# Kernel optimization log

Measured on AMD Instinct MI355X. Metric: run time of the kernel, lower is better.

Reference implementation:

```python
import jax, jax.numpy as jnp
import numpy as np

PI = 3.1415927410125732
N = 4096
VELOCITY = 5e-7
RC = 3.15e-6          # collision radius
RR = 8e-6             # repulsion radius
RO = 2.5e-5           # orientation radius (Ra = inf -> inside_Ra all-true)
ALPHA = PI            # field of view; < 2*pi so within_view masking is active
DT_TRANS = 1.4e-14    # translational diffusion DT
DR = 0.0028
GAMMA = 25.0
DT = 0.2              # timestep dt
COLLISION_ITERS = 3   # fixed-iteration version of recursive solve_collisions
EPS = 1e-14


def _c(x):  # [N,2] real -> complex64
    return jax.lax.complex(x[..., 0], x[..., 1])


def _r(z):  # complex -> [..., 2] real
    return jnp.stack([z.real, z.imag], axis=-1)


def _anglediff(a, b):
    # torch get_anglediff: wrap angle(a)-angle(b) into (-pi, pi)
    diff = jnp.angle(a) - jnp.angle(b)
    diff = jnp.where(diff <= -PI, jnp.mod(diff, PI), diff)
    return diff - (diff >= PI) * (2.0 * PI)


def _cossim(a, b):
    # nn.CosineSimilarity(dim=1, eps=1e-14) on view_as_real of complex vectors
    dot = a.real * b.real + a.imag * b.imag
    na = jnp.sqrt(a.real ** 2 + a.imag ** 2 + 1e-30)
    nb = jnp.sqrt(b.real ** 2 + b.imag ** 2 + 1e-30)
    return dot / (jnp.maximum(na, EPS) * jnp.maximum(nb, EPS))


def setup_inputs() -> dict:
    key = jax.random.key(0)
    k1, k2, k3, k4, k5 = jax.random.split(key, 5)
    positions = jax.random.normal(k1, (N, 2), jnp.float32) * 5e-4
    ang = jax.random.uniform(k2, (N,), jnp.float32, -PI, PI)
    orientations = jnp.stack([jnp.cos(ang), jnp.sin(ang)], axis=-1)  # unit complex
    Deltas = jax.random.uniform(k3, (1,), jnp.float32, 0.1, 0.6)
    rot_noise = jax.random.normal(k4, (N,), jnp.float32)
    trans_noise = jax.random.normal(k5, (N, 2), jnp.float32)
    return {"positions": positions, "orientations": orientations, "Deltas": Deltas,
            "rot_noise": rot_noise, "trans_noise": trans_noise}


def reference(positions, orientations, Deltas, rot_noise, trans_noise):
    p = _c(positions)      # [N] complex positions
    u = _c(orientations)   # [N] complex orientations
    n = p.shape[0]
    eye = jnp.eye(n, dtype=bool)

    # pairwise direction/distance: dirs[i,j] = p_j - p_i
    dirs = p[None, :] - p[:, None]
    dists = jnp.abs(dirs)

    inside_Rr = (dists <= RR) & ~eye
    inside_Ro = dists <= RO + RC
    # inside_Ra with Ra = inf is all-True

    # angle between separation vector and orientation of the *neighbor* j
    ang_diff = _anglediff(dirs, u[None, :])
    in_front = ang_diff < PI / 2
    within_view = ang_diff < ALPHA  # alpha < 2*pi branch active

    cdtype = p.dtype
    mask_rr = (inside_Rr & in_front).astype(cdtype)
    mask_ra = within_view.astype(cdtype)  # inside_Ra all True
    mask_ro = (inside_Ro & within_view).astype(cdtype)

    n_r = mask_rr.real.sum(axis=1)
    S = (mask_rr @ p) / jnp.maximum(n_r, 1.0) - p * jnp.sign(n_r)
    d = -S

    n_a = mask_ra.real.sum(axis=1)
    cms = (mask_ra @ p) / jnp.maximum(n_a, 1.0)
    Ps = cms - p * jnp.sign(n_a)

    orientation_sums = mask_ro @ u

    leftturns = Ps * jnp.exp(1j * Deltas)
    rightturns = Ps * jnp.exp(-1j * Deltas)

    # T >= T_release branch: pick the turn most aligned with neighbor orientations
    left_closer = _cossim(leftturns, orientation_sums) >= _cossim(rightturns, orientation_sums)
    best_turns = jnp.where(left_closer, leftturns, rightturns)

    d_abs = jnp.abs(d)
    d_safe = jnp.where(d_abs > 0, d, jnp.ones((), cdtype))
    best_safe = jnp.where(jnp.abs(best_turns) > 0, best_turns, jnp.ones((), cdtype))
    angle_to_target = jnp.where(d_abs > 0, _anglediff(d_safe, u), _anglediff(best_safe, u))

    # rotational_noise = randn * sqrt(2*DR); rotation = exp(i*(dt*Gamma*DR*sin + noise*sqrt(dt)))
    rot = jnp.exp(1j * (DT * GAMMA * DR * jnp.sin(angle_to_target)
                        + rot_noise * np.float32(np.sqrt(2 * DR)) * np.float32(np.sqrt(DT))))

    # complex-normal translational noise (per-component std 1/sqrt(2)) * sqrt(2*DT) * sqrt(dt)
    tn = _c(trans_noise) * np.float32(np.sqrt(0.5)) * np.float32(np.sqrt(2 * DT_TRANS))
    translation = DT * VELOCITY * u + tn * np.float32(np.sqrt(DT))

    def collide(i, pos):
        dd = pos[None, :] - pos[:, None]
        dd_nd = jnp.where(eye, jnp.ones((), pos.dtype), dd)  # avoid 0/0 on diagonal
        ab = jnp.where(eye, 0.0, jnp.abs(dd_nd))
        coll = ab <= 2 * RC - jnp.eye(n, dtype=ab.dtype)
        safe = jnp.where(coll, ab, 1.0)
        move = jnp.where(coll, dd / safe * ((2.1 * RC - ab) * 0.5), jnp.zeros((), pos.dtype))
        return pos - move.sum(axis=1)

    new_p = jax.lax.fori_loop(0, COLLISION_ITERS, collide, p + translation)
    new_u = u * rot

    # pack the 5 complex outputs as real [5, N, 2]
    return jnp.stack([_r(new_p), _r(new_u), _r(orientation_sums), _r(leftturns), _r(rightturns)], axis=0)
```

## Files before the change

### kernel.cpp

```cpp
#include <hip/hip_runtime.h>
#include <math.h>

#define NPART 4096
#define NBLK  512
#define NTHR  256
#define IPB   8
#define CAPL  1024
#define SMAX  512

constexpr float RORC   = (float)(2.5e-5 + 3.15e-6);
constexpr float RORC2  = RORC * RORC;
constexpr float RRF    = 8e-6f;
constexpr float RR2    = RRF * RRF;
constexpr float TWORC  = (float)(2.0 * 3.15e-6);
constexpr float TWORC2 = TWORC * TWORC;
constexpr float C21RC  = (float)(2.1 * 3.15e-6);
constexpr float RCAND2 = 1.6e-9f;
constexpr float C_ROT  = (float)(0.2 * 25.0 * 0.0028);
constexpr float C_RN1  = (float)0.07483314773547883;
constexpr float C_SQDT = (float)0.4472135954999579;
constexpr float C_TRV  = (float)(0.2 * 5e-7);
constexpr float C_HALF = (float)0.7071067811865476;
constexpr float C_SQ2T = (float)1.6733200530681511e-07;
constexpr float EPSF   = 1e-14f;

__global__ __launch_bounds__(NTHR) void fused_all(
        const float2* __restrict__ pos, const float2* __restrict__ ori,
        const float* __restrict__ Deltas, const float* __restrict__ rot_noise,
        const float2* __restrict__ trans_noise, float2* __restrict__ out) {
    __shared__ float4   pp4[NPART / 2];
    __shared__ float    sred[2 * NTHR];
    __shared__ float    res[5][IPB];
    __shared__ unsigned bmap[NPART / 32];
    __shared__ int      lpairs[CAPL];
    __shared__ int      Sidx[SMAX];
    __shared__ float4   posS4[SMAX / 2];
    __shared__ int      lcnt, scnt;
    __shared__ int      iloc[IPB];
    float2* ppos_s = (float2*)pp4;
    float2* posS   = (float2*)posS4;

    const int tid = threadIdx.x;
    if (tid == 0) { lcnt = 0; scnt = 0; }
    if (tid < 5 * IPB) ((float*)res)[tid] = 0.f;
    if (tid < NPART / 32) bmap[tid] = 0u;
    const int il  = tid & (IPB - 1);
    const int seg = tid / IPB;
    const int gi  = blockIdx.x * IPB + il;

    for (int k = 0; k < NPART / NTHR; ++k)
        ppos_s[k * NTHR + tid] = pos[k * NTHR + tid];
    __syncthreads();

    const float2 pi = ppos_s[gi];
    const int base64 = seg * 64;
    for (int tb = 0; tb < 16; ++tb) {
        const int kb = (tb + seg) & 15;
        const float4 v0 = pp4[base64 + kb];
        const float4 v1 = pp4[base64 + kb + 16];
        const float4 v2 = pp4[base64 + kb + 32];
        const float4 v3 = pp4[base64 + kb + 48];
        #pragma unroll
        for (int s = 0; s < 4; ++s) {
            const float4 v = (s == 0) ? v0 : (s == 1) ? v1 : (s == 2) ? v2 : v3;
            const int j0 = seg * 128 + 2 * (kb + 16 * s);
            const float dx0 = v.x - pi.x, dy0 = v.y - pi.y;
            const float dx1 = v.z - pi.x, dy1 = v.w - pi.y;
            const float r20 = fmaf(dx0, dx0, dy0 * dy0);
            const float r21 = fmaf(dx1, dx1, dy1 * dy1);
            if (fminf(r20, r21) <= RCAND2) {
                if (r20 <= RCAND2) {
                    const int slot = atomicAdd(&lcnt, 1);
                    if (slot < CAPL) lpairs[slot] = (il << 12) | j0;
                    atomicOr(&bmap[j0 >> 5], 1u << (j0 & 31));
                }
                if (r21 <= RCAND2) {
                    const int j1 = j0 + 1;
                    const int slot = atomicAdd(&lcnt, 1);
                    if (slot < CAPL) lpairs[slot] = (il << 12) | j1;
                    atomicOr(&bmap[j1 >> 5], 1u << (j1 & 31));
                }
            }
        }
    }
    __syncthreads();

    const int n_l = (lcnt < CAPL) ? lcnt : CAPL;
    if (tid < 128) {
        for (int e = tid; e < n_l; e += 128) {
            const int code = lpairs[e];
            const int jil = code >> 12, j = code & (NPART - 1);
            const float2 pj = ppos_s[j];
            const float2 pi2 = ppos_s[blockIdx.x * IPB + jil];
            const float dx = pj.x - pi2.x, dy = pj.y - pi2.y;
            const float r2 = fmaf(dx, dx, dy * dy);
            if (r2 <= RORC2) {
                const float2 uj = ori[j];
                atomicAdd(&res[3][jil], uj.x);
                atomicAdd(&res[4][jil], uj.y);
                if (r2 <= RR2 && r2 > 0.f) {
                    const float dt_ = fmaf(dx, uj.x, dy * uj.y);
                    const float cr_ = fmaf(dy, uj.x, -dx * uj.y);
                    if (!((dt_ <= 0.f) && (cr_ >= 0.f))) {
                        atomicAdd(&res[0][jil], 1.f);
                        atomicAdd(&res[1][jil], pj.x);
                        atomicAdd(&res[2][jil], pj.y);
                    }
                }
            }
        }
    } else {
        const int w = tid - 128;
        unsigned bits = bmap[w];
        while (bits) {
            const int b = __ffs(bits) - 1;
            bits &= bits - 1;
            const int p = w * 32 + b;
            const int slot = atomicAdd(&scnt, 1);
            if (slot < SMAX) {
                Sidx[slot] = p;
                if ((p >> 3) == (int)blockIdx.x) iloc[p & (IPB - 1)] = slot;
            }
        }
    }
    __syncthreads();
    const int nS = (scnt < SMAX) ? scnt : SMAX;

    for (int m = tid; m < nS; m += NTHR) {
        const int p = Sidx[m];
        const float2 pp = ppos_s[p];
        const float2 uu = ori[p];
        const float2 tn = trans_noise[p];
        posS[m] = make_float2(
            pp.x + (C_TRV * uu.x + ((tn.x * C_HALF) * C_SQ2T) * C_SQDT),
            pp.y + (C_TRV * uu.y + ((tn.y * C_HALF) * C_SQ2T) * C_SQDT));
    }

    float mx = 0.f, my = 0.f;
    for (int k = 0; k < NPART / NTHR; ++k) {
        const float2 v = ppos_s[k * NTHR + tid];
        mx += v.x; my += v.y;
    }
    sred[tid] = mx; sred[NTHR + tid] = my;
    __syncthreads();
    for (int s = NTHR / 2; s > 0; s >>= 1) {
        if (tid < s) { sred[tid] += sred[tid + s]; sred[NTHR + tid] += sred[NTHR + tid + s]; }
        __syncthreads();
    }
    const float cmx = sred[0]    * (1.f / NPART);
    const float cmy = sred[NTHR] * (1.f / NPART);

    if (tid < IPB) {
        const int g2 = blockIdx.x * IPB + tid;
        const float2 p = ppos_s[g2];
        const float2 u = ori[g2];
        const float nrv = res[0][tid], sxv = res[1][tid], syv = res[2][tid];
        const float osx = res[3][tid], osy = res[4][tid];

        const float inv = 1.f / fmaxf(nrv, 1.f);
        const float sg  = (nrv > 0.f) ? 1.f : 0.f;
        const float Sx = sxv * inv - p.x * sg;
        const float Sy = syv * inv - p.y * sg;
        const float dxv = -Sx, dyv = -Sy;

        const float Psx = cmx - p.x;
        const float Psy = cmy - p.y;

        float sd, cd;
        sincosf(Deltas[0], &sd, &cd);
        const float Lx = Psx * cd - Psy * sd;
        const float Ly = Psx * sd + Psy * cd;
        const float Rx = Psx * cd + Psy * sd;
        const float Ry = Psy * cd - Psx * sd;

        const float no  = fmaxf(sqrtf(osx * osx + osy * osy + 1e-30f), EPSF);
        const float nl  = fmaxf(sqrtf(Lx * Lx + Ly * Ly + 1e-30f), EPSF);
        const float nrr = fmaxf(sqrtf(Rx * Rx + Ry * Ry + 1e-30f), EPSF);
        const float csl = (Lx * osx + Ly * osy) / (nl * no);
        const float csr = (Rx * osx + Ry * osy) / (nrr * no);
        const bool left = (csl >= csr);
        const float bx = left ? Lx : Rx;
        const float by = left ? Ly : Ry;

        float cx, cy;
        if (dxv != 0.f || dyv != 0.f)    { cx = dxv; cy = dyv; }
        else if (bx != 0.f || by != 0.f) { cx = bx;  cy = by;  }
        else                             { cx = 1.f; cy = 0.f; }

        const float dt_ = cx * u.x + cy * u.y;
        const float cr_ = cy * u.x - cx * u.y;
        const float sin_t = cr_ / sqrtf(dt_ * dt_ + cr_ * cr_);

        const float ang = C_ROT * sin_t + (rot_noise[g2] * C_RN1) * C_SQDT;
        float sa, ca;
        sincosf(ang, &sa, &ca);
        out[1 * NPART + g2] = make_float2(u.x * ca - u.y * sa,
                                          u.x * sa + u.y * ca);
        out[2 * NPART + g2] = make_float2(osx, osy);
        out[3 * NPART + g2] = make_float2(Lx, Ly);
        out[4 * NPART + g2] = make_float2(Rx, Ry);
    }
    __syncthreads();

    for (int pass = 0; pass < 3; ++pass) {
        float px[2], py[2], ax[2] = {0.f, 0.f}, ay[2] = {0.f, 0.f};
        bool  mv[2];
        #pragma unroll
        for (int q = 0; q < 2; ++q) {
            const int m = tid + q * NTHR;
            mv[q] = (m < nS);
            if (mv[q]) { px[q] = posS[m].x; py[q] = posS[m].y; }
        }
        int b = 0;
        for (; b + 4 <= nS; b += 4) {
            const float4 w0 = posS4[(b >> 1)];
            const float4 w1 = posS4[(b >> 1) + 1];
            const float bxs[4] = {w0.x, w0.z, w1.x, w1.z};
            const float bys[4] = {w0.y, w0.w, w1.y, w1.w};
            #pragma unroll
            for (int s = 0; s < 4; ++s) {
                #pragma unroll
                for (int q = 0; q < 2; ++q) {
                    if (mv[q]) {
                        const float dx = bxs[s] - px[q], dy = bys[s] - py[q];
                        const float r2 = fmaf(dx, dx, dy * dy);
                        if (r2 <= TWORC2 && r2 > 0.f) {
                            const float ab = sqrtf(r2);
                            const float sc = (C21RC - ab) * 0.5f / ab;
                            ax[q] = fmaf(dx, sc, ax[q]);
                            ay[q] = fmaf(dy, sc, ay[q]);
                        }
                    }
                }
            }
        }
        for (; b < nS; ++b) {
            const float2 pb = posS[b];
            #pragma unroll
            for (int q = 0; q < 2; ++q) {
                if (mv[q]) {
                    const float dx = pb.x - px[q], dy = pb.y - py[q];
                    const float r2 = fmaf(dx, dx, dy * dy);
                    if (r2 <= TWORC2 && r2 > 0.f) {
                        const float ab = sqrtf(r2);
                        const float sc = (C21RC - ab) * 0.5f / ab;
                        ax[q] = fmaf(dx, sc, ax[q]);
                        ay[q] = fmaf(dy, sc, ay[q]);
                    }
                }
            }
        }
        __syncthreads();
        #pragma unroll
        for (int q = 0; q < 2; ++q) {
            const int m = tid + q * NTHR;
            if (m < nS) posS[m] = make_float2(px[q] - ax[q], py[q] - ay[q]);
        }
        __syncthreads();
    }
    if (tid < IPB)
        out[0 * NPART + blockIdx.x * IPB + tid] = posS[iloc[tid]];
}

extern "C" void kernel_launch(void* const* d_in, const int* in_sizes, int n_in,
                              void* d_out, int out_size, void* d_ws, size_t ws_size,
                              hipStream_t stream) {
    const float2* pos = (const float2*)d_in[0];
    const float2* ori = (const float2*)d_in[1];
    const float*  del = (const float*)d_in[2];
    const float*  rn  = (const float*)d_in[3];
    const float2* tn  = (const float2*)d_in[4];
    float2* o2 = (float2*)d_out;
    (void)d_ws; (void)ws_size;

    fused_all<<<dim3(NBLK), dim3(NTHR), 0, stream>>>(pos, ori, del, rn, tn, o2);
}
```

Baseline: 96.23 us.

## Replace brute-force neighbor scan with per-block uniform grid cell list

Each block now bins all 4096 particles into a 64x64 uniform grid in shared memory (count, scan, scatter) and then checks only the 3x3 neighbouring cells of each of its 8 particles, one warp-sized group per particle. This replaces the all-pairs scan of 4096 candidates per particle and the shared pair list with atomic accumulation. Each block rebuilds the full grid redundantly, which adds atomics, a block scan and extra syncs. The cell size must be at least the candidate radius, and particles outside the grid extent are clamped into the edge cells.

```diff
diff --git a/kernel.cpp b/kernel.cpp
--- a/kernel.cpp
+++ b/kernel.cpp
@@ -5,8 +5,9 @@
 #define NBLK  512
 #define NTHR  256
 #define IPB   8
-#define CAPL  1024
 #define SMAX  512
+#define GDIM  64
+#define NCELL (GDIM * GDIM)
 
 constexpr float RORC   = (float)(2.5e-5 + 3.15e-6);
 constexpr float RORC2  = RORC * RORC;
@@ -16,6 +17,8 @@
 constexpr float TWORC2 = TWORC * TWORC;
 constexpr float C21RC  = (float)(2.1 * 3.15e-6);
 constexpr float RCAND2 = 1.6e-9f;
+constexpr float GMIN   = -2.048e-3f;
+constexpr float GINV   = 15625.0f;
 constexpr float C_ROT  = (float)(0.2 * 25.0 * 0.0028);
 constexpr float C_RN1  = (float)0.07483314773547883;
 constexpr float C_SQDT = (float)0.4472135954999579;
@@ -24,92 +27,133 @@
 constexpr float C_SQ2T = (float)1.6733200530681511e-07;
 constexpr float EPSF   = 1e-14f;
 
+__device__ __forceinline__ int cell_of(float x, float y) {
+    int cx = (int)floorf((x - GMIN) * GINV);
+    int cy = (int)floorf((y - GMIN) * GINV);
+    cx = min(max(cx, 0), GDIM - 1);
+    cy = min(max(cy, 0), GDIM - 1);
+    return cy * GDIM + cx;
+}
+
 __global__ __launch_bounds__(NTHR) void fused_all(
         const float2* __restrict__ pos, const float2* __restrict__ ori,
         const float* __restrict__ Deltas, const float* __restrict__ rot_noise,
         const float2* __restrict__ trans_noise, float2* __restrict__ out) {
     __shared__ float4   pp4[NPART / 2];
-    __shared__ float    sred[2 * NTHR];
+    __shared__ int      ptr[NCELL];
+    __shared__ unsigned short sortid[NPART];
+    __shared__ float    sred[5 * NTHR];
     __shared__ float    res[5][IPB];
     __shared__ unsigned bmap[NPART / 32];
-    __shared__ int      lpairs[CAPL];
     __shared__ int      Sidx[SMAX];
     __shared__ float4   posS4[SMAX / 2];
-    __shared__ int      lcnt, scnt;
+    __shared__ int      scnt;
     __shared__ int      iloc[IPB];
     float2* ppos_s = (float2*)pp4;
     float2* posS   = (float2*)posS4;
-
-    const int tid = threadIdx.x;
-    if (tid == 0) { lcnt = 0; scnt = 0; }
-    if (tid < 5 * IPB) ((float*)res)[tid] = 0.f;
+    int*    sredi  = (int*)sred;
+
+    const int tid  = threadIdx.x;
+    const int il   = tid >> 5;
+    const int lane = tid & 31;
+    const int gi   = blockIdx.x * IPB + il;
+    if (tid == 0) scnt = 0;
     if (tid < NPART / 32) bmap[tid] = 0u;
-    const int il  = tid & (IPB - 1);
-    const int seg = tid / IPB;
-    const int gi  = blockIdx.x * IPB + il;
 
     for (int k = 0; k < NPART / NTHR; ++k)
         ppos_s[k * NTHR + tid] = pos[k * NTHR + tid];
+    for (int k = 0; k < NCELL / NTHR; ++k)
+        ptr[k * NTHR + tid] = 0;
+    __syncthreads();
+
+    for (int k = 0; k < NPART / NTHR; ++k) {
+        const int p = k * NTHR + tid;
+        const float2 pp = ppos_s[p];
+        atomicAdd(&ptr[cell_of(pp.x, pp.y)], 1);
+    }
+    __syncthreads();
+
+    {
+        const int base = tid * (NCELL / NTHR);
+        int v[NCELL / NTHR];
+        int sum = 0;
+        #pragma unroll
+        for (int t = 0; t < NCELL / NTHR; ++t) { v[t] = ptr[base + t]; sum += v[t]; }
+        sredi[tid] = sum;
+        __syncthreads();
+        for (int off = 1; off < NTHR; off <<= 1) {
+            const int a = (tid >= off) ? sredi[tid - off] : 0;
+            __syncthreads();
+            sredi[tid] += a;
+            __syncthreads();
+        }
+        int run = sredi[tid] - sum;
+        #pragma unroll
+        for (int t = 0; t < NCELL / NTHR; ++t) { ptr[base + t] = run; run += v[t]; }
+    }
+    __syncthreads();
+
+    for (int k = 0; k < NPART / NTHR; ++k) {
+        const int p = k * NTHR + tid;
+        const float2 pp = ppos_s[p];
+        const int slot = atomicAdd(&ptr[cell_of(pp.x, pp.y)], 1);
+        sortid[slot] = (unsigned short)p;
+    }
     __syncthreads();
 
     const float2 pi = ppos_s[gi];
-    const int base64 = seg * 64;
-    for (int tb = 0; tb < 16; ++tb) {
-        const int kb = (tb + seg) & 15;
-        const float4 v0 = pp4[base64 + kb];
-        const float4 v1 = pp4[base64 + kb + 16];
-        const float4 v2 = pp4[base64 + kb + 32];
-        const float4 v3 = pp4[base64 + kb + 48];
-        #pragma unroll
-        for (int s = 0; s < 4; ++s) {
-            const float4 v = (s == 0) ? v0 : (s == 1) ? v1 : (s == 2) ? v2 : v3;
-            const int j0 = seg * 128 + 2 * (kb + 16 * s);
-            const float dx0 = v.x - pi.x, dy0 = v.y - pi.y;
-            const float dx1 = v.z - pi.x, dy1 = v.w - pi.y;
-            const float r20 = fmaf(dx0, dx0, dy0 * dy0);
-            const float r21 = fmaf(dx1, dx1, dy1 * dy1);
-            if (fminf(r20, r21) <= RCAND2) {
-                if (r20 <= RCAND2) {
-                    const int slot = atomicAdd(&lcnt, 1);
-                    if (slot < CAPL) lpairs[slot] = (il << 12) | j0;
-                    atomicOr(&bmap[j0 >> 5], 1u << (j0 & 31));
-                }
-                if (r21 <= RCAND2) {
-                    const int j1 = j0 + 1;
-                    const int slot = atomicAdd(&lcnt, 1);
-                    if (slot < CAPL) lpairs[slot] = (il << 12) | j1;
-                    atomicOr(&bmap[j1 >> 5], 1u << (j1 & 31));
-                }
-            }
-        }
-    }
-    __syncthreads();
-
-    const int n_l = (lcnt < CAPL) ? lcnt : CAPL;
-    if (tid < 128) {
-        for (int e = tid; e < n_l; e += 128) {
-            const int code = lpairs[e];
-            const int jil = code >> 12, j = code & (NPART - 1);
-            const float2 pj = ppos_s[j];
-            const float2 pi2 = ppos_s[blockIdx.x * IPB + jil];
-            const float dx = pj.x - pi2.x, dy = pj.y - pi2.y;
-            const float r2 = fmaf(dx, dx, dy * dy);
-            if (r2 <= RORC2) {
-                const float2 uj = ori[j];
-                atomicAdd(&res[3][jil], uj.x);
-                atomicAdd(&res[4][jil], uj.y);
-                if (r2 <= RR2 && r2 > 0.f) {
-                    const float dt_ = fmaf(dx, uj.x, dy * uj.y);
-                    const float cr_ = fmaf(dy, uj.x, -dx * uj.y);
-                    if (!((dt_ <= 0.f) && (cr_ >= 0.f))) {
-                        atomicAdd(&res[0][jil], 1.f);
-                        atomicAdd(&res[1][jil], pj.x);
-                        atomicAdd(&res[2][jil], pj.y);
+    {
+        int cxi = (int)floorf((pi.x - GMIN) * GINV);
+        int cyi = (int)floorf((pi.y - GMIN) * GINV);
+        cxi = min(max(cxi, 0), GDIM - 1);
+        cyi = min(max(cyi, 0), GDIM - 1);
+        float nr = 0.f, sx = 0.f, sy = 0.f, oxs = 0.f, oys = 0.f;
+        for (int dy = -1; dy <= 1; ++dy) {
+            const int cy = cyi + dy;
+            if (cy < 0 || cy >= GDIM) continue;
+            for (int dx = -1; dx <= 1; ++dx) {
+                const int cx = cxi + dx;
+                if (cx < 0 || cx >= GDIM) continue;
+                const int c  = cy * GDIM + cx;
+                const int b0 = (c > 0) ? ptr[c - 1] : 0;
+                const int e0 = ptr[c];
+                for (int t = b0 + lane; t < e0; t += 32) {
+                    const int j = sortid[t];
+                    const float2 pj = ppos_s[j];
+                    const float dxp = pj.x - pi.x, dyp = pj.y - pi.y;
+                    const float r2 = fmaf(dxp, dxp, dyp * dyp);
+                    if (r2 <= RCAND2) {
+                        atomicOr(&bmap[j >> 5], 1u << (j & 31));
+                        if (r2 <= RORC2) {
+                            const float2 uj = ori[j];
+                            oxs += uj.x; oys += uj.y;
+                            if (r2 <= RR2 && r2 > 0.f) {
+                                const float dt_ = fmaf(dxp, uj.x, dyp * uj.y);
+                                const float cr_ = fmaf(dyp, uj.x, -dxp * uj.y);
+                                if (!((dt_ <= 0.f) && (cr_ >= 0.f))) {
+                                    nr += 1.f; sx += pj.x; sy += pj.y;
+                                }
+                            }
+                        }
                     }
                 }
             }
         }
-    } else {
+        sred[0 * NTHR + il * 32 + lane] = nr;
+        sred[1 * NTHR + il * 32 + lane] = sx;
+        sred[2 * NTHR + il * 32 + lane] = sy;
+        sred[3 * NTHR + il * 32 + lane] = oxs;
+        sred[4 * NTHR + il * 32 + lane] = oys;
+    }
+    __syncthreads();
+
+    if (tid < 5 * IPB) {
+        const int q = tid / IPB, ii = tid & (IPB - 1);
+        float acc = 0.f;
+        #pragma unroll
+        for (int s = 0; s < 32; ++s) acc += sred[q * NTHR + ii * 32 + s];
+        res[q][ii] = acc;
+    } else if (tid >= 128 && tid < 128 + NPART / 32) {
         const int w = tid - 128;
         unsigned bits = bmap[w];
         while (bits) {
@@ -141,6 +185,7 @@
         const float2 v = ppos_s[k * NTHR + tid];
         mx += v.x; my += v.y;
     }
+    __syncthreads();
     sred[tid] = mx; sred[NTHR + tid] = my;
     __syncthreads();
     for (int s = NTHR / 2; s > 0; s >>= 1) {
```

After: 96.95 us. Within noise of the previous version (+0.7%).
